# Kernel tuning notes

Hardware: AMD Instinct MI355X
Metric: run time of the kernel (lower is better)

## Reference

```python
import jax, jax.numpy as jnp
import numpy as np

N, M, D_IN, D_K = 2048, 1024, 128, 64


def setup_inputs() -> dict:
    key = jax.random.key(0)
    kq, kk, kw = jax.random.split(key, 3)
    q = jax.random.normal(kq, (N, D_IN), dtype=jnp.float32)
    k = jax.random.normal(kk, (M, D_IN), dtype=jnp.float32)
    # glorot-uniform init for the bias-free Linear(d_in -> d_k) weight [d_k, d_in]
    limit = np.sqrt(6.0 / (D_IN + D_K)).astype(np.float32)
    W = jax.random.uniform(kw, (D_K, D_IN), dtype=jnp.float32, minval=-limit, maxval=limit)
    return {"q": q, "k": k, "W": W}


def reference(q, k, W):
    # pairwise broadcast difference: [n, m, d_in]
    diff = q[:, None, :] - k[None, :, :]
    # linear projection (nn.Linear: x @ W.T): [n, m, d_k]
    proj = jnp.einsum("nmd,kd->nmk", diff, W)
    # L2 norm over last dim: [n, m]
    dist = jnp.sqrt(jnp.sum(proj * proj, axis=-1))
    score = -dist * 0.5
    # masked_softmax with mask=None over dim=-1 == plain softmax over m
    return jax.nn.softmax(score, axis=-1)
```

## Files before the change

### kernel.cpp

```cpp
#include <hip/hip_runtime.h>
#include <hip/hip_bf16.h>
#include <math.h>

#define N_Q 2048
#define M_K 1024
#define DIN 128
#define DK  64

typedef __attribute__((ext_vector_type(8))) short short8;
typedef __attribute__((ext_vector_type(4))) float f32x4;
typedef __attribute__((ext_vector_type(4))) unsigned int u32x4;

__global__ __launch_bounds__(256) void proj_kernel(
    const float* __restrict__ q, const float* __restrict__ k,
    const float* __restrict__ W,
    unsigned int* __restrict__ Qhl, unsigned int* __restrict__ Khl,
    float* __restrict__ qn2, float* __restrict__ kn2)
{
    __shared__ float W_lds[DK][DIN + 4];
    __shared__ float row_lds[4][DIN];
    const int tx = threadIdx.x;

    const float4* W4 = (const float4*)W;
    #pragma unroll
    for (int i = 0; i < 8; ++i) {
        int idx = tx + i * 256;
        float4 v = W4[idx];
        int r = idx >> 5, c = (idx & 31) * 4;
        *(float4*)&W_lds[r][c] = v;
    }

    const int wave = tx >> 6, lane = tx & 63;
    const int row  = blockIdx.x * 4 + wave;
    const float* src = (row < N_Q) ? (q + (size_t)row * DIN)
                                   : (k + (size_t)(row - N_Q) * DIN);
    row_lds[wave][lane]      = src[lane];
    row_lds[wave][lane + 64] = src[lane + 64];
    __syncthreads();

    float acc = 0.f;
    #pragma unroll
    for (int d = 0; d < DIN; d += 4) {
        float4 wv = *(const float4*)&W_lds[lane][d];
        float4 rv = *(const float4*)&row_lds[wave][d];
        acc = fmaf(wv.x, rv.x, acc);
        acc = fmaf(wv.y, rv.y, acc);
        acc = fmaf(wv.z, rv.z, acc);
        acc = fmaf(wv.w, rv.w, acc);
    }

    float sq = acc * acc;
    #pragma unroll
    for (int off = 32; off >= 1; off >>= 1)
        sq += __shfl_xor(sq, off, 64);

    __hip_bfloat16 hb = __float2bfloat16(acc);
    float hf = __bfloat162float(hb);
    __hip_bfloat16 lb = __float2bfloat16(acc - hf);
    unsigned int packed = (unsigned int)(*(unsigned short*)&hb)
                        | ((unsigned int)(*(unsigned short*)&lb) << 16);

    if (row < N_Q) {
        Qhl[(size_t)row * DK + lane] = packed;
        if (lane == 0) qn2[row] = sq;
    } else {
        const int m = row - N_Q;
        Khl[(size_t)m * DK + lane] = packed;
        if (lane == 0) kn2[m] = sq;
    }
}

static __device__ __forceinline__ void unpack8(const unsigned int* __restrict__ p,
                                               short8& h, short8& l)
{
    u32x4 a = *(const u32x4*)p;
    u32x4 b = *(const u32x4*)(p + 4);
    u32x4 hu, lu;
    hu.x = (a.x & 0xFFFFu) | (a.y << 16);
    hu.y = (a.z & 0xFFFFu) | (a.w << 16);
    hu.z = (b.x & 0xFFFFu) | (b.y << 16);
    hu.w = (b.z & 0xFFFFu) | (b.w << 16);
    lu.x = (a.x >> 16) | (a.y & 0xFFFF0000u);
    lu.y = (a.z >> 16) | (a.w & 0xFFFF0000u);
    lu.z = (b.x >> 16) | (b.y & 0xFFFF0000u);
    lu.w = (b.z >> 16) | (b.w & 0xFFFF0000u);
    union { u32x4 u; short8 s; } ch, cl;
    ch.u = hu; cl.u = lu;
    h = ch.s; l = cl.s;
}

__global__ __launch_bounds__(512) void score_kernel(
    const unsigned int* __restrict__ Qhl, const unsigned int* __restrict__ Khl,
    const float* __restrict__ qn2, const float* __restrict__ kn2,
    float* __restrict__ out)
{
    __shared__ float redmax[16][8];
    __shared__ float redsum[16][8];

    const int tx = threadIdx.x;
    const int w = tx >> 6, l = tx & 63;
    const int g = l >> 4, c = l & 15;
    const int n0 = blockIdx.x * 16;

    const unsigned int* qr = Qhl + (size_t)(n0 + c) * DK;
    short8 Ah0, Al0, Ah1, Al1;
    unpack8(qr + g * 8, Ah0, Al0);
    unpack8(qr + 32 + g * 8, Ah1, Al1);

    float qn[4];
    #pragma unroll
    for (int j = 0; j < 4; ++j) qn[j] = qn2[n0 + 4 * g + j];

    float s[8][4];
    #pragma unroll
    for (int t = 0; t < 8; ++t) {
        const int m = w * 128 + t * 16 + c;
        const unsigned int* kr = Khl + (size_t)m * DK;
        short8 Bh0, Bl0, Bh1, Bl1;
        unpack8(kr + g * 8, Bh0, Bl0);
        unpack8(kr + 32 + g * 8, Bh1, Bl1);

        f32x4 acc = {0.f, 0.f, 0.f, 0.f};
        acc = __builtin_amdgcn_mfma_f32_16x16x32_bf16(Ah0, Bh0, acc, 0, 0, 0);
        acc = __builtin_amdgcn_mfma_f32_16x16x32_bf16(Ah1, Bh1, acc, 0, 0, 0);
        acc = __builtin_amdgcn_mfma_f32_16x16x32_bf16(Ah0, Bl0, acc, 0, 0, 0);
        acc = __builtin_amdgcn_mfma_f32_16x16x32_bf16(Ah1, Bl1, acc, 0, 0, 0);
        acc = __builtin_amdgcn_mfma_f32_16x16x32_bf16(Al0, Bh0, acc, 0, 0, 0);
        acc = __builtin_amdgcn_mfma_f32_16x16x32_bf16(Al1, Bh1, acc, 0, 0, 0);

        const float kn = kn2[m];
        #pragma unroll
        for (int j = 0; j < 4; ++j) {
            float d2 = fmaxf(qn[j] + kn - 2.f * acc[j], 0.f);
            s[t][j] = -0.5f * sqrtf(d2);
        }
    }

    #pragma unroll
    for (int j = 0; j < 4; ++j) {
        float m8 = s[0][j];
        #pragma unroll
        for (int t = 1; t < 8; ++t) m8 = fmaxf(m8, s[t][j]);
        m8 = fmaxf(m8, __shfl_xor(m8, 1, 64));
        m8 = fmaxf(m8, __shfl_xor(m8, 2, 64));
        m8 = fmaxf(m8, __shfl_xor(m8, 4, 64));
        m8 = fmaxf(m8, __shfl_xor(m8, 8, 64));
        if (c == 0) redmax[4 * g + j][w] = m8;
    }
    __syncthreads();

    float mx[4];
    #pragma unroll
    for (int j = 0; j < 4; ++j) {
        float m = redmax[4 * g + j][0];
        #pragma unroll
        for (int ww = 1; ww < 8; ++ww) m = fmaxf(m, redmax[4 * g + j][ww]);
        mx[j] = m;
    }

    #pragma unroll
    for (int j = 0; j < 4; ++j) {
        float t8 = 0.f;
        #pragma unroll
        for (int t = 0; t < 8; ++t) {
            s[t][j] = __expf(s[t][j] - mx[j]);
            t8 += s[t][j];
        }
        t8 += __shfl_xor(t8, 1, 64);
        t8 += __shfl_xor(t8, 2, 64);
        t8 += __shfl_xor(t8, 4, 64);
        t8 += __shfl_xor(t8, 8, 64);
        if (c == 0) redsum[4 * g + j][w] = t8;
    }
    __syncthreads();

    float inv[4];
    #pragma unroll
    for (int j = 0; j < 4; ++j) {
        float t = 0.f;
        #pragma unroll
        for (int ww = 0; ww < 8; ++ww) t += redsum[4 * g + j][ww];
        inv[j] = 1.0f / t;
    }

    #pragma unroll
    for (int t = 0; t < 8; ++t) {
        const int m = w * 128 + t * 16 + c;
        #pragma unroll
        for (int j = 0; j < 4; ++j)
            out[(size_t)(n0 + 4 * g + j) * M_K + m] = s[t][j] * inv[j];
    }
}

extern "C" void kernel_launch(void* const* d_in, const int* in_sizes, int n_in,
                              void* d_out, int out_size, void* d_ws, size_t ws_size,
                              hipStream_t stream)
{
    const float* q = (const float*)d_in[0];
    const float* k = (const float*)d_in[1];
    const float* W = (const float*)d_in[2];
    float* out = (float*)d_out;

    unsigned char* base = (unsigned char*)d_ws;
    unsigned int* Qhl = (unsigned int*)(base);
    unsigned int* Khl = (unsigned int*)(base + 524288);
    float* qn2 = (float*)(base + 786432);
    float* kn2 = (float*)(base + 794624);

    proj_kernel<<<(N_Q + M_K) / 4, 256, 0, stream>>>(q, k, W, Qhl, Khl, qn2, kn2);
    score_kernel<<<N_Q / 16, 512, 0, stream>>>(Qhl, Khl, qn2, kn2, out);
}
```

Measured before the change: 24.96 us.

## Fuse projection and score kernels with an atomic grid-wide barrier

```diff
diff --git a/kernel.cpp b/kernel.cpp
--- a/kernel.cpp
+++ b/kernel.cpp
@@ -6,71 +6,22 @@
 #define M_K 1024
 #define DIN 128
 #define DK  64
+#define NBLK 256
 
 typedef __attribute__((ext_vector_type(8))) short short8;
 typedef __attribute__((ext_vector_type(4))) float f32x4;
 typedef __attribute__((ext_vector_type(4))) unsigned int u32x4;
 
-__global__ __launch_bounds__(256) void proj_kernel(
-    const float* __restrict__ q, const float* __restrict__ k,
-    const float* __restrict__ W,
-    unsigned int* __restrict__ Qhl, unsigned int* __restrict__ Khl,
-    float* __restrict__ qn2, float* __restrict__ kn2)
-{
-    __shared__ float W_lds[DK][DIN + 4];
-    __shared__ float row_lds[4][DIN];
-    const int tx = threadIdx.x;
-
-    const float4* W4 = (const float4*)W;
-    #pragma unroll
-    for (int i = 0; i < 8; ++i) {
-        int idx = tx + i * 256;
-        float4 v = W4[idx];
-        int r = idx >> 5, c = (idx & 31) * 4;
-        *(float4*)&W_lds[r][c] = v;
-    }
-
-    const int wave = tx >> 6, lane = tx & 63;
-    const int row  = blockIdx.x * 4 + wave;
-    const float* src = (row < N_Q) ? (q + (size_t)row * DIN)
-                                   : (k + (size_t)(row - N_Q) * DIN);
-    row_lds[wave][lane]      = src[lane];
-    row_lds[wave][lane + 64] = src[lane + 64];
-    __syncthreads();
-
-    float acc = 0.f;
-    #pragma unroll
-    for (int d = 0; d < DIN; d += 4) {
-        float4 wv = *(const float4*)&W_lds[lane][d];
-        float4 rv = *(const float4*)&row_lds[wave][d];
-        acc = fmaf(wv.x, rv.x, acc);
-        acc = fmaf(wv.y, rv.y, acc);
-        acc = fmaf(wv.z, rv.z, acc);
-        acc = fmaf(wv.w, rv.w, acc);
-    }
-
-    float sq = acc * acc;
-    #pragma unroll
-    for (int off = 32; off >= 1; off >>= 1)
-        sq += __shfl_xor(sq, off, 64);
-
-    __hip_bfloat16 hb = __float2bfloat16(acc);
+static __device__ __forceinline__ unsigned int pack_split(float v)
+{
+    __hip_bfloat16 hb = __float2bfloat16(v);
     float hf = __bfloat162float(hb);
-    __hip_bfloat16 lb = __float2bfloat16(acc - hf);
-    unsigned int packed = (unsigned int)(*(unsigned short*)&hb)
-                        | ((unsigned int)(*(unsigned short*)&lb) << 16);
-
-    if (row < N_Q) {
-        Qhl[(size_t)row * DK + lane] = packed;
-        if (lane == 0) qn2[row] = sq;
-    } else {
-        const int m = row - N_Q;
-        Khl[(size_t)m * DK + lane] = packed;
-        if (lane == 0) kn2[m] = sq;
-    }
-}
-
-static __device__ __forceinline__ void unpack8(const unsigned int* __restrict__ p,
+    __hip_bfloat16 lb = __float2bfloat16(v - hf);
+    return (unsigned int)(*(unsigned short*)&hb)
+         | ((unsigned int)(*(unsigned short*)&lb) << 16);
+}
+
+static __device__ __forceinline__ void unpack8(const unsigned int* p,
                                                short8& h, short8& l)
 {
     u32x4 a = *(const u32x4*)p;
@@ -89,27 +40,87 @@
     h = ch.s; l = cl.s;
 }
 
-__global__ __launch_bounds__(512) void score_kernel(
-    const unsigned int* __restrict__ Qhl, const unsigned int* __restrict__ Khl,
-    const float* __restrict__ qn2, const float* __restrict__ kn2,
-    float* __restrict__ out)
-{
-    __shared__ float redmax[16][8];
-    __shared__ float redsum[16][8];
+__global__ __launch_bounds__(512) void fused_kernel(
+    const float* __restrict__ q, const float* __restrict__ k,
+    const float* __restrict__ W,
+    unsigned int* __restrict__ Khl, float* __restrict__ kn2,
+    unsigned int* __restrict__ ctr, float* __restrict__ out)
+{
+    __shared__ float W_lds[DK][DIN + 4];
+    __shared__ float row_lds[8][2][DIN];
+    __shared__ unsigned int qhl_lds[8][DK];
+    __shared__ float qn2_lds[8];
+    __shared__ float redmax[8][8];
+    __shared__ float redsum[8][8];
 
     const int tx = threadIdx.x;
-    const int w = tx >> 6, l = tx & 63;
-    const int g = l >> 4, c = l & 15;
-    const int n0 = blockIdx.x * 16;
-
-    const unsigned int* qr = Qhl + (size_t)(n0 + c) * DK;
+    const int w = tx >> 6, lane = tx & 63;
+    const int bid = blockIdx.x;
+
+    const float4* W4 = (const float4*)W;
+    #pragma unroll
+    for (int i = 0; i < 4; ++i) {
+        int idx = tx + i * 512;
+        float4 v = W4[idx];
+        *(float4*)&W_lds[idx >> 5][(idx & 31) * 4] = v;
+    }
+
+    const int qrow = bid * 8 + w;
+    const int krow = (bid & 127) * 8 + w;
+    {
+        const float* qs = q + (size_t)qrow * DIN;
+        const float* ks = k + (size_t)krow * DIN;
+        row_lds[w][0][lane]      = qs[lane];
+        row_lds[w][0][lane + 64] = qs[lane + 64];
+        row_lds[w][1][lane]      = ks[lane];
+        row_lds[w][1][lane + 64] = ks[lane + 64];
+    }
+    __syncthreads();
+
+    float aq = 0.f, ak = 0.f;
+    #pragma unroll
+    for (int d = 0; d < DIN; d += 4) {
+        float4 wv = *(const float4*)&W_lds[lane][d];
+        float4 rq = *(const float4*)&row_lds[w][0][d];
+        float4 rk = *(const float4*)&row_lds[w][1][d];
+        aq = fmaf(wv.x, rq.x, aq); aq = fmaf(wv.y, rq.y, aq);
+        aq = fmaf(wv.z, rq.z, aq); aq = fmaf(wv.w, rq.w, aq);
+        ak = fmaf(wv.x, rk.x, ak); ak = fmaf(wv.y, rk.y, ak);
+        ak = fmaf(wv.z, rk.z, ak); ak = fmaf(wv.w, rk.w, ak);
+    }
+
+    float sqq = aq * aq, sqk = ak * ak;
+    #pragma unroll
+    for (int off = 32; off >= 1; off >>= 1) {
+        sqq += __shfl_xor(sqq, off, 64);
+        sqk += __shfl_xor(sqk, off, 64);
+    }
+
+    qhl_lds[w][lane] = pack_split(aq);
+    if (lane == 0) qn2_lds[w] = sqq;
+    Khl[(size_t)krow * DK + lane] = pack_split(ak);
+    if (lane == 0) kn2[krow] = sqk;
+
+    __syncthreads();
+    if (tx == 0) {
+        __threadfence();
+        __hip_atomic_fetch_add(ctr, 1u, __ATOMIC_ACQ_REL, __HIP_MEMORY_SCOPE_AGENT);
+        while (__hip_atomic_load(ctr, __ATOMIC_ACQUIRE, __HIP_MEMORY_SCOPE_AGENT)
+               < (unsigned)NBLK)
+            __builtin_amdgcn_s_sleep(8);
+    }
+    __syncthreads();
+
+    const int g = lane >> 4, c = lane & 15;
+    const int n0 = bid * 8;
+
     short8 Ah0, Al0, Ah1, Al1;
-    unpack8(qr + g * 8, Ah0, Al0);
-    unpack8(qr + 32 + g * 8, Ah1, Al1);
+    unpack8(&qhl_lds[c & 7][g * 8],      Ah0, Al0);
+    unpack8(&qhl_lds[c & 7][32 + g * 8], Ah1, Al1);
 
     float qn[4];
     #pragma unroll
-    for (int j = 0; j < 4; ++j) qn[j] = qn2[n0 + 4 * g + j];
+    for (int j = 0; j < 4; ++j) qn[j] = qn2_lds[(4 * g + j) & 7];
 
     float s[8][4];
     #pragma unroll
@@ -145,16 +156,17 @@
         m8 = fmaxf(m8, __shfl_xor(m8, 2, 64));
         m8 = fmaxf(m8, __shfl_xor(m8, 4, 64));
         m8 = fmaxf(m8, __shfl_xor(m8, 8, 64));
-        if (c == 0) redmax[4 * g + j][w] = m8;
+        if (c == 0 && g < 2) redmax[4 * g + j][w] = m8;
     }
     __syncthreads();
 
     float mx[4];
     #pragma unroll
     for (int j = 0; j < 4; ++j) {
-        float m = redmax[4 * g + j][0];
-        #pragma unroll
-        for (int ww = 1; ww < 8; ++ww) m = fmaxf(m, redmax[4 * g + j][ww]);
+        const float* rm = redmax[(4 * g + j) & 7];
+        float m = rm[0];
+        #pragma unroll
+        for (int ww = 1; ww < 8; ++ww) m = fmaxf(m, rm[ww]);
         mx[j] = m;
     }
 
@@ -170,25 +182,27 @@
         t8 += __shfl_xor(t8, 2, 64);
         t8 += __shfl_xor(t8, 4, 64);
         t8 += __shfl_xor(t8, 8, 64);
-        if (c == 0) redsum[4 * g + j][w] = t8;
-    }
-    __syncthreads();
-
-    float inv[4];
-    #pragma unroll
-    for (int j = 0; j < 4; ++j) {
-        float t = 0.f;
-        #pragma unroll
-        for (int ww = 0; ww < 8; ++ww) t += redsum[4 * g + j][ww];
-        inv[j] = 1.0f / t;
-    }
-
-    #pragma unroll
-    for (int t = 0; t < 8; ++t) {
-        const int m = w * 128 + t * 16 + c;
-        #pragma unroll
-        for (int j = 0; j < 4; ++j)
-            out[(size_t)(n0 + 4 * g + j) * M_K + m] = s[t][j] * inv[j];
+        if (c == 0 && g < 2) redsum[4 * g + j][w] = t8;
+    }
+    __syncthreads();
+
+    if (g < 2) {
+        float inv[4];
+        #pragma unroll
+        for (int j = 0; j < 4; ++j) {
+            const float* rs = redsum[4 * g + j];
+            float t = 0.f;
+            #pragma unroll
+            for (int ww = 0; ww < 8; ++ww) t += rs[ww];
+            inv[j] = 1.0f / t;
+        }
+        #pragma unroll
+        for (int t = 0; t < 8; ++t) {
+            const int m = w * 128 + t * 16 + c;
+            #pragma unroll
+            for (int j = 0; j < 4; ++j)
+                out[(size_t)(n0 + 4 * g + j) * M_K + m] = s[t][j] * inv[j];
+        }
     }
 }
 
@@ -202,11 +216,10 @@
     float* out = (float*)d_out;
 
     unsigned char* base = (unsigned char*)d_ws;
-    unsigned int* Qhl = (unsigned int*)(base);
-    unsigned int* Khl = (unsigned int*)(base + 524288);
-    float* qn2 = (float*)(base + 786432);
-    float* kn2 = (float*)(base + 794624);
-
-    proj_kernel<<<(N_Q + M_K) / 4, 256, 0, stream>>>(q, k, W, Qhl, Khl, qn2, kn2);
-    score_kernel<<<N_Q / 16, 512, 0, stream>>>(Qhl, Khl, qn2, kn2, out);
-}
+    unsigned int* Khl = (unsigned int*)base;
+    float* kn2 = (float*)(base + 262144);
+    unsigned int* ctr = (unsigned int*)(base + 524288);
+
+    hipMemsetAsync(ctr, 0, 4, stream);
+    fused_kernel<<<NBLK, 512, 0, stream>>>(q, k, W, Khl, kn2, ctr, out);
+}
```

Measured after the change: 40.39 us. +61.8%, slower.
